# Kernel tuning notes

Measured on AMD Instinct MI355X. Metric: run time of the kernel, lower is better.

The kernel has to match this reference:

```python
import jax, jax.numpy as jnp
import numpy as np

HIDDEN = 1024
NUM_HEADS = 8
HEAD_DIM = HIDDEN // NUM_HEADS
ROPE_BASE = 10000.0
RMS_EPS = 1e-6


def _rotate_half(x):
    # interleaved rotate: (x0,x1,x2,x3,...) -> (-x1,x0,-x3,x2,...)
    x1 = x[..., ::2]
    x2 = x[..., 1::2]
    return jnp.stack([-x2, x1], axis=-1).reshape(x.shape)


def _rope_cos_sin(seq_len, rotary_dim, dtype):
    inv_freq = 1.0 / (ROPE_BASE ** (jnp.arange(0, rotary_dim, 2, dtype=jnp.float32) / rotary_dim))
    pos = jnp.arange(seq_len, dtype=jnp.float32)
    freqs = pos[:, None] * inv_freq[None, :]            # [S, rd/2]
    cos = jnp.repeat(jnp.cos(freqs), 2, axis=-1)        # [S, rd]
    sin = jnp.repeat(jnp.sin(freqs), 2, axis=-1)
    return cos.astype(dtype)[None, None], sin.astype(dtype)[None, None]


def setup_inputs() -> dict:
    key = jax.random.key(0)
    k = jax.random.split(key, 8)
    B, S, H = 2, 2048, HIDDEN
    hidden_states = jax.random.normal(k[0], (B, S, H), dtype=jnp.float32)
    attention_mask = jax.random.randint(k[1], (B, S, S), 0, 2) > 0
    rel_ts_bias = jax.random.normal(k[2], (B, S, S), dtype=jnp.float32)
    s1 = 1.0 / np.sqrt(H)
    W_qkvu = jax.random.normal(k[3], (H, H * 6), dtype=jnp.float32) * s1
    W_out = jax.random.normal(k[4], (H * 3, H), dtype=jnp.float32) * (1.0 / np.sqrt(H * 3))
    b_out = jnp.zeros((H,), dtype=jnp.float32)
    rms_weight = jnp.ones((H,), dtype=jnp.float32)
    return {"hidden_states": hidden_states, "attention_mask": attention_mask,
            "rel_ts_bias": rel_ts_bias, "W_qkvu": W_qkvu, "W_out": W_out,
            "b_out": b_out, "rms_weight": rms_weight}


def reference(hidden_states, attention_mask, rel_ts_bias, W_qkvu, W_out, b_out, rms_weight):
    B, S, H = hidden_states.shape
    nh, hd = NUM_HEADS, HEAD_DIM
    fused = jax.nn.silu(hidden_states @ W_qkvu)          # [B,S,6H]
    gated = fused[..., :3 * H]                            # [B,S,3H]
    v = fused[..., 3 * H:4 * H].reshape(B, S, nh, hd).transpose(0, 2, 1, 3)
    q = fused[..., 4 * H:5 * H].reshape(B, S, nh, hd).transpose(0, 2, 1, 3)
    kk = fused[..., 5 * H:].reshape(B, S, nh, hd).transpose(0, 2, 1, 3)

    cos, sin = _rope_cos_sin(S, hd, hidden_states.dtype)  # rotary_dim == head_dim
    q_rope = q * cos + _rotate_half(q) * sin
    k_rope = kk * cos + _rotate_half(kk) * sin

    inv_s = 1.0 / max(S, 1)
    qk = jax.nn.relu(jnp.einsum('bhnd,bhmd->bhnm', q, kk)) * inv_s
    qk_rope = jax.nn.relu(jnp.einsum('bhnd,bhmd->bhnm', q_rope, k_rope)) * inv_s

    mask = attention_mask[:, None]                        # [B,1,S,S]
    qk = jnp.where(mask, qk, 0.0)
    qk_rope = jnp.where(mask, qk_rope, 0.0)
    ts_bias = jnp.where(attention_mask, rel_ts_bias, 0.0)

    ts_out = jnp.einsum('bnm,bhmd->bnhd', ts_bias, v)
    rope_out = jnp.einsum('bhnm,bhmd->bnhd', qk_rope, v)
    plain_out = jnp.einsum('bhnm,bhmd->bnhd', qk, v)

    combined = jnp.concatenate([rope_out, ts_out, plain_out], axis=-1).reshape(B, S, 3 * H)
    out = (combined * gated) @ W_out + b_out
    y = out + hidden_states
    rms = jax.lax.rsqrt(jnp.mean(y * y, axis=-1, keepdims=True) + RMS_EPS)
    return y * rms * rms_weight
```

## Files before the change

### kernel.cpp

```cpp
#include <hip/hip_runtime.h>
#include <math.h>

static constexpr int Bz = 2;
static constexpr int Sq = 2048;
static constexpr int Hh = 1024;
static constexpr int NH = 8;
static constexpr int HD = 128;
static constexpr int H3 = 3072;
static constexpr int H6 = 6144;

typedef unsigned short ushort_t;
typedef float f32x4v __attribute__((ext_vector_type(4)));
typedef float f32x16v __attribute__((ext_vector_type(16)));
typedef short s16x8 __attribute__((ext_vector_type(8)));

static constexpr size_t FUSED_OFF = 0;
static constexpr size_t A2_OFF    = 12582912;
static constexpr size_t HB_OFF    = 18874368;
static constexpr size_t MTB_OFF   = 18874368;
static constexpr size_t WQT_OFF   = 20971520;
static constexpr size_t WOT_OFF   = 24117248;
static constexpr size_t QR_OFF    = 25690112;
static constexpr size_t KR_OFF    = 27787264;
static constexpr size_t VT_OFF    = 29884416;
static constexpr size_t TAB_OFF   = 31981568;
static constexpr size_t FLAG_OFF  = 32243712;
static constexpr size_t TSB_OFF   = 32243716;

__device__ __forceinline__ float silu_(float x) { return x / (1.0f + expf(-x)); }
__device__ __forceinline__ ushort_t f2bf(float x) {
  unsigned int u = __float_as_uint(x);
  u += 0x7fffu + ((u >> 16) & 1u);
  return (ushort_t)(u >> 16);
}
__device__ __forceinline__ float bf2f(ushort_t u) {
  return __uint_as_float(((unsigned int)u) << 16);
}
__device__ __forceinline__ void g2l16(const ushort_t* g, ushort_t* l) {
  __builtin_amdgcn_global_load_lds(
      (const __attribute__((address_space(1))) unsigned int*)g,
      (__attribute__((address_space(3))) unsigned int*)l, 16, 0, 0);
}

__global__ __launch_bounds__(256) void hstu_mask_detect(const unsigned int* __restrict__ m,
                                                        int* __restrict__ flag) {
  __shared__ int s_any;
  if (threadIdx.x == 0) s_any = 0;
  __syncthreads();
  int any = 0;
  for (int i = threadIdx.x; i < 65536; i += 256)
    if (m[i] > 1u) any = 1;
  if (any) s_any = 1;
  __syncthreads();
  if (threadIdx.x == 0) *flag = s_any;
}

__global__ __launch_bounds__(256) void hstu_tab(float* __restrict__ tab) {
  int t = blockIdx.x * 256 + threadIdx.x;
  int i = t & 63;
  int s = t >> 6;
  float inv = powf(10000.0f, -(float)i / 64.0f);
  float sn, cs;
  sincosf((float)s * inv, &sn, &cs);
  tab[2 * t + 0] = cs;
  tab[2 * t + 1] = sn;
}

__global__ __launch_bounds__(256) void hstu_msk(const int* __restrict__ mask32,
                                                const unsigned char* __restrict__ mask8,
                                                const int* __restrict__ mflag,
                                                const float* __restrict__ bias,
                                                ushort_t* __restrict__ tsb,
                                                unsigned char* __restrict__ mtb8) {
  const size_t base = ((size_t)blockIdx.x * 256 + threadIdx.x) * 8;
  const int m_u8 = *mflag;
  int mk[8];
  if (m_u8) {
    uchar4 a = *(const uchar4*)&mask8[base];
    uchar4 b = *(const uchar4*)&mask8[base + 4];
    mk[0] = a.x; mk[1] = a.y; mk[2] = a.z; mk[3] = a.w;
    mk[4] = b.x; mk[5] = b.y; mk[6] = b.z; mk[7] = b.w;
  } else {
    int4 a = *(const int4*)&mask32[base];
    int4 b = *(const int4*)&mask32[base + 4];
    mk[0] = a.x; mk[1] = a.y; mk[2] = a.z; mk[3] = a.w;
    mk[4] = b.x; mk[5] = b.y; mk[6] = b.z; mk[7] = b.w;
  }
  float4 b0 = *(const float4*)&bias[base];
  float4 b1 = *(const float4*)&bias[base + 4];
  float bb[8] = {b0.x, b0.y, b0.z, b0.w, b1.x, b1.y, b1.z, b1.w};
  ushort_t ts[8];
  unsigned char mo[8];
#pragma unroll
  for (int i = 0; i < 8; ++i) {
    ts[i] = f2bf(mk[i] ? bb[i] : 0.0f);
    mo[i] = mk[i] ? 1u : 0u;
  }
  *(s16x8*)&tsb[base] = *(s16x8*)ts;
  *(uint2*)&mtb8[base] = *(uint2*)mo;
}

__global__ __launch_bounds__(256) void hstu_cvt(const float* __restrict__ in,
                                                ushort_t* __restrict__ out, int n4) {
  int i = blockIdx.x * 256 + threadIdx.x;
  if (i >= n4) return;
  float4 v = *(const float4*)&in[(size_t)i * 4];
  ushort4 o;
  o.x = f2bf(v.x); o.y = f2bf(v.y); o.z = f2bf(v.z); o.w = f2bf(v.w);
  *(ushort4*)&out[(size_t)i * 4] = o;
}

__global__ __launch_bounds__(256) void hstu_cvt_t(const float* __restrict__ in,
                                                  ushort_t* __restrict__ out, int K, int N) {
  __shared__ float t[32][33];
  const int n0 = blockIdx.x * 32, k0 = blockIdx.y * 32;
  const int c = threadIdx.x & 31, rr = threadIdx.x >> 5;
#pragma unroll
  for (int p = 0; p < 4; ++p)
    t[rr + p * 8][c] = in[(size_t)(k0 + rr + p * 8) * N + n0 + c];
  __syncthreads();
#pragma unroll
  for (int p = 0; p < 4; ++p)
    out[(size_t)(n0 + rr + p * 8) * K + k0 + c] = f2bf(t[c][rr + p * 8]);
}

__global__ __launch_bounds__(256) void hstu_rope(const ushort_t* __restrict__ fused,
                                                 const float2* __restrict__ tab,
                                                 ushort_t* __restrict__ qr,
                                                 ushort_t* __restrict__ kr) {
  const int idx = blockIdx.x * 256 + threadIdx.x;
  const int row = idx >> 7;
  const int cg = (idx & 127) * 8;
  const int s = row & (Sq - 1);
  const float2* trow = &tab[(size_t)s * 64 + ((cg & 127) >> 1)];
  float2 t[4];
#pragma unroll
  for (int p = 0; p < 4; ++p) t[p] = trow[p];

  s16x8 q8 = *(const s16x8*)&fused[(size_t)row * H6 + 4 * Hh + cg];
  s16x8 k8 = *(const s16x8*)&fused[(size_t)row * H6 + 5 * Hh + cg];
  ushort_t qo[8], ko[8];
#pragma unroll
  for (int p = 0; p < 4; ++p) {
    float qx = bf2f((ushort_t)q8[2 * p]), qy = bf2f((ushort_t)q8[2 * p + 1]);
    float kx = bf2f((ushort_t)k8[2 * p]), ky = bf2f((ushort_t)k8[2 * p + 1]);
    qo[2 * p] = f2bf(qx * t[p].x - qy * t[p].y);
    qo[2 * p + 1] = f2bf(qy * t[p].x + qx * t[p].y);
    ko[2 * p] = f2bf(kx * t[p].x - ky * t[p].y);
    ko[2 * p + 1] = f2bf(ky * t[p].x + kx * t[p].y);
  }
  *(s16x8*)&qr[(size_t)row * Hh + cg] = *(s16x8*)qo;
  *(s16x8*)&kr[(size_t)row * Hh + cg] = *(s16x8*)ko;
}

__global__ __launch_bounds__(256) void hstu_vt(const ushort_t* __restrict__ fused,
                                               ushort_t* __restrict__ vt) {
  __shared__ ushort_t t[32][36];
  const int m0 = blockIdx.x * 32, d0 = blockIdx.y * 32, bh = blockIdx.z;
  const int b = bh >> 3, h = bh & 7;
  const int r = threadIdx.x >> 3, cg = (threadIdx.x & 7) * 4;
  *(ushort4*)&t[r][cg] =
      *(const ushort4*)&fused[(size_t)(b * Sq + m0 + r) * H6 + 3 * Hh + h * HD + d0 + cg];
  __syncthreads();
  ushort4 o;
  o.x = t[cg + 0][r]; o.y = t[cg + 1][r]; o.z = t[cg + 2][r]; o.w = t[cg + 3][r];
  *(ushort4*)&vt[(size_t)(bh * HD + d0 + r) * Sq + m0 + cg] = o;
}

__global__ __launch_bounds__(256) void hstu_gemm_silu(const ushort_t* __restrict__ A,
                                                      const ushort_t* __restrict__ Bt,
                                                      ushort_t* __restrict__ C) {
  constexpr int K = 1024, N = H6;
  __shared__ ushort_t As[128 * 64];
  __shared__ ushort_t Bs[128 * 64];
  const int tid = threadIdx.x, lane = tid & 63, wid = tid >> 6;
  const int lo4 = lane & 15, hi2 = lane >> 4;
  const int wr = wid >> 1, wc = wid & 1;
  const int row0 = blockIdx.y * 128, col0 = blockIdx.x * 128;
  const int srow = lane >> 3, scol = (lane & 7) * 8;
  f32x4v acc[4][4];
#pragma unroll
  for (int i = 0; i < 4; ++i)
#pragma unroll
    for (int j = 0; j < 4; ++j) acc[i][j] = {0.f, 0.f, 0.f, 0.f};

  for (int k0 = 0; k0 < K; k0 += 64) {
    __syncthreads();
#pragma unroll
    for (int i = 0; i < 4; ++i) {
      const int rb = wid * 32 + i * 8;
      g2l16(&A[(size_t)(row0 + rb + srow) * K + k0 + scol], &As[rb * 64]);
      g2l16(&Bt[(size_t)(col0 + rb + srow) * K + k0 + scol], &Bs[rb * 64]);
    }
    __syncthreads();
#pragma unroll
    for (int kc = 0; kc < 2; ++kc) {
      s16x8 af[4], bfr[4];
#pragma unroll
      for (int mi = 0; mi < 4; ++mi)
        af[mi] = *(const s16x8*)&As[(wr * 64 + mi * 16 + lo4) * 64 + kc * 32 + hi2 * 8];
#pragma unroll
      for (int nj = 0; nj < 4; ++nj)
        bfr[nj] = *(const s16x8*)&Bs[(wc * 64 + nj * 16 + lo4) * 64 + kc * 32 + hi2 * 8];
#pragma unroll
      for (int mi = 0; mi < 4; ++mi)
#pragma unroll
        for (int nj = 0; nj < 4; ++nj)
          acc[mi][nj] = __builtin_amdgcn_mfma_f32_16x16x32_bf16(af[mi], bfr[nj], acc[mi][nj], 0, 0, 0);
    }
  }
#pragma unroll
  for (int mi = 0; mi < 4; ++mi)
#pragma unroll
    for (int nj = 0; nj < 4; ++nj)
#pragma unroll
      for (int r = 0; r < 4; ++r) {
        const int row = row0 + wr * 64 + mi * 16 + hi2 * 4 + r;
        const int col = col0 + wc * 64 + nj * 16 + lo4;
        C[(size_t)row * N + col] = f2bf(silu_(acc[mi][nj][r]));
      }
}

__global__ __launch_bounds__(256) void hstu_gemm_out(const ushort_t* __restrict__ A,
                                                     const ushort_t* __restrict__ Bt,
                                                     const float* __restrict__ bout,
                                                     const float* __restrict__ hidden,
                                                     float* __restrict__ C) {
  constexpr int K = H3, N = Hh;
  __shared__ ushort_t As[128 * 64];
  __shared__ ushort_t Bs[64 * 64];
  const int tid = threadIdx.x, lane = tid & 63, wid = tid >> 6;
  const int lo4 = lane & 15, hi2 = lane >> 4;
  const int wr = wid >> 1, wc = wid & 1;
  const int row0 = blockIdx.y * 128, col0 = blockIdx.x * 64;
  const int srow = lane >> 3, scol = (lane & 7) * 8;
  f32x4v acc[4][2];
#pragma unroll
  for (int i = 0; i < 4; ++i)
#pragma unroll
    for (int j = 0; j < 2; ++j) acc[i][j] = {0.f, 0.f, 0.f, 0.f};

  for (int k0 = 0; k0 < K; k0 += 64) {
    __syncthreads();
#pragma unroll
    for (int i = 0; i < 4; ++i) {
      const int rb = wid * 32 + i * 8;
      g2l16(&A[(size_t)(row0 + rb + srow) * K + k0 + scol], &As[rb * 64]);
    }
#pragma unroll
    for (int i = 0; i < 2; ++i) {
      const int rb = wid * 16 + i * 8;
      g2l16(&Bt[(size_t)(col0 + rb + srow) * K + k0 + scol], &Bs[rb * 64]);
    }
    __syncthreads();
#pragma unroll
    for (int kc = 0; kc < 2; ++kc) {
      s16x8 af[4], bfr[2];
#pragma unroll
      for (int mi = 0; mi < 4; ++mi)
        af[mi] = *(const s16x8*)&As[(wr * 64 + mi * 16 + lo4) * 64 + kc * 32 + hi2 * 8];
#pragma unroll
      for (int nj = 0; nj < 2; ++nj)
        bfr[nj] = *(const s16x8*)&Bs[(wc * 32 + nj * 16 + lo4) * 64 + kc * 32 + hi2 * 8];
#pragma unroll
      for (int mi = 0; mi < 4; ++mi)
#pragma unroll
        for (int nj = 0; nj < 2; ++nj)
          acc[mi][nj] = __builtin_amdgcn_mfma_f32_16x16x32_bf16(af[mi], bfr[nj], acc[mi][nj], 0, 0, 0);
    }
  }
#pragma unroll
  for (int mi = 0; mi < 4; ++mi)
#pragma unroll
    for (int nj = 0; nj < 2; ++nj)
#pragma unroll
      for (int r = 0; r < 4; ++r) {
        const int row = row0 + wr * 64 + mi * 16 + hi2 * 4 + r;
        const int col = col0 + wc * 32 + nj * 16 + lo4;
        C[(size_t)row * N + col] = acc[mi][nj][r] + bout[col] + hidden[(size_t)row * N + col];
      }
}

__global__ __launch_bounds__(512, 4) void hstu_attn(const ushort_t* __restrict__ fused,
                                                    const ushort_t* __restrict__ qr,
                                                    const ushort_t* __restrict__ kr,
                                                    const ushort_t* __restrict__ vt,
                                                    const ushort_t* __restrict__ tsb,
                                                    const unsigned char* __restrict__ mtb8,
                                                    ushort_t* __restrict__ a2) {
  __shared__ __align__(16) ushort_t Ks[64][136];
  __shared__ __align__(16) ushort_t KRs[64][136];
  __shared__ __align__(16) ushort_t Vt[128][72];
  __shared__ __align__(16) ushort_t Pl[2][64][72];
  __shared__ __align__(16) unsigned char Mt[64][72];

  const int tid = threadIdx.x;
  const int lane = tid & 63;
  const int wid = tid >> 6;
  const int l31 = lane & 31;
  const int khalf = lane >> 5;
  const int h = blockIdx.x;
  const int n0 = blockIdx.y * 64;
  const int b = blockIdx.z;
  const float ivs = 1.0f / 2048.0f;
  constexpr int NT = Sq / 64;

  const int t_w = wid >> 2;
  const int nq = (wid >> 1) & 1;
  const int mq = wid & 1;
  const int nh = wid & 1;
  const int dq = wid >> 1;

#define STAGE_QQR()                                                              \
  {                                                                              \
    _Pragma("unroll") for (int p = 0; p < 2; ++p) {                              \
      const int row = (tid >> 4) + p * 32;                                       \
      const int col = (tid & 15) * 8;                                            \
      const size_t gr = (size_t)(b * Sq + n0 + row);                             \
      *(s16x8*)&Ks[row][col] = *(const s16x8*)&fused[gr * H6 + 4 * Hh + h * HD + col]; \
      *(s16x8*)&KRs[row][col] = *(const s16x8*)&qr[gr * Hh + h * HD + col];      \
    }                                                                            \
  }
#define STAGE_KKR(T)                                                             \
  {                                                                              \
    _Pragma("unroll") for (int p = 0; p < 2; ++p) {                              \
      const int row = (tid >> 4) + p * 32;                                       \
      const int col = (tid & 15) * 8;                                            \
      const size_t gr = (size_t)(b * Sq + (T) * 64 + row);                       \
      *(s16x8*)&Ks[row][col] = *(const s16x8*)&fused[gr * H6 + 5 * Hh + h * HD + col]; \
      *(s16x8*)&KRs[row][col] = *(const s16x8*)&kr[gr * Hh + h * HD + col];      \
    }                                                                            \
  }
#define STAGE_MT(T)                                                              \
  {                                                                              \
    const int row = tid >> 3;                                                    \
    const int c8 = (tid & 7) * 8;                                                \
    *(uint2*)&Mt[row][c8] =                                                      \
        *(const uint2*)&mtb8[(size_t)(b * Sq + n0 + row) * Sq + (T) * 64 + c8];  \
  }
#define STAGE_VT(T)                                                              \
  {                                                                              \
    _Pragma("unroll") for (int p = 0; p < 2; ++p) {                              \
      const int dd = (tid >> 3) + p * 64;                                        \
      const int mcol = (tid & 7) * 8;                                            \
      *(s16x8*)&Vt[dd][mcol] =                                                   \
          *(const s16x8*)&vt[(size_t)((b * NH + h) * HD + dd) * Sq + (T) * 64 + mcol]; \
    }                                                                            \
  }

  STAGE_QQR();
  __syncthreads();
  s16x8 qf[8];
  {
    const ushort_t(*Qsrc)[136] = t_w ? KRs : Ks;
#pragma unroll
    for (int ks = 0; ks < 8; ++ks)
      qf[ks] = *(const s16x8*)&Qsrc[nq * 32 + l31][ks * 16 + khalf * 8];
  }
  __syncthreads();
  STAGE_KKR(0);
  STAGE_MT(0);
  __syncthreads();

  f32x16v acc0 = {0.f, 0.f, 0.f, 0.f, 0.f, 0.f, 0.f, 0.f,
                  0.f, 0.f, 0.f, 0.f, 0.f, 0.f, 0.f, 0.f};
  f32x16v acc1 = acc0;
  f32x16v acc2 = acc0;

  const size_t tsrow = (size_t)(b * Sq + n0 + nh * 32 + l31) * Sq;

  for (int t = 0; t < NT; ++t) {
    const int m0 = t * 64;
    STAGE_VT(t);
    s16x8 tsf[4];
#pragma unroll
    for (int ks = 0; ks < 4; ++ks)
      tsf[ks] = *(const s16x8*)&tsb[tsrow + m0 + ks * 16 + khalf * 8];
    {
      const ushort_t(*Kmat)[136] = t_w ? KRs : Ks;
      f32x16v sacc = {0.f, 0.f, 0.f, 0.f, 0.f, 0.f, 0.f, 0.f,
                      0.f, 0.f, 0.f, 0.f, 0.f, 0.f, 0.f, 0.f};
#pragma unroll
      for (int ks = 0; ks < 8; ++ks) {
        s16x8 bfr = *(const s16x8*)&Kmat[mq * 32 + l31][ks * 16 + khalf * 8];
        sacc = __builtin_amdgcn_mfma_f32_32x32x16_bf16(qf[ks], bfr, sacc, 0, 0, 0);
      }
      const int m = mq * 32 + l31;
#pragma unroll
      for (int r = 0; r < 16; ++r) {
        const int n = nq * 32 + (r & 3) + 8 * (r >> 2) + 4 * khalf;
        const float val = Mt[n][m] ? fmaxf(sacc[r], 0.f) * ivs : 0.f;
        Pl[t_w][n][m] = f2bf(val);
      }
    }
    __syncthreads();
    if (t + 1 < NT) {
      STAGE_KKR(t + 1);
      STAGE_MT(t + 1);
    }
#pragma unroll
    for (int ks = 0; ks < 4; ++ks) {
      s16x8 bV = *(const s16x8*)&Vt[dq * 32 + l31][ks * 16 + khalf * 8];
      s16x8 aP0 = *(const s16x8*)&Pl[0][nh * 32 + l31][ks * 16 + khalf * 8];
      s16x8 aP1 = *(const s16x8*)&Pl[1][nh * 32 + l31][ks * 16 + khalf * 8];
      acc0 = __builtin_amdgcn_mfma_f32_32x32x16_bf16(aP0, bV, acc0, 0, 0, 0);
      acc1 = __builtin_amdgcn_mfma_f32_32x32x16_bf16(aP1, bV, acc1, 0, 0, 0);
      acc2 = __builtin_amdgcn_mfma_f32_32x32x16_bf16(tsf[ks], bV, acc2, 0, 0, 0);
    }
    __syncthreads();
  }
#undef STAGE_QQR
#undef STAGE_KKR
#undef STAGE_MT
#undef STAGE_VT

  const int dd = dq * 32 + l31;
#pragma unroll
  for (int r = 0; r < 16; ++r) {
    const int n = n0 + nh * 32 + (r & 3) + 8 * (r >> 2) + 4 * khalf;
    const size_t rowb = (size_t)(b * Sq + n);
    const int c_pl = h * 384 + 256 + dd;
    const int c_ro = h * 384 + 0 + dd;
    const int c_ts = h * 384 + 128 + dd;
    a2[rowb * H3 + c_pl] = f2bf(acc0[r] * bf2f(fused[rowb * H6 + c_pl]));
    a2[rowb * H3 + c_ro] = f2bf(acc1[r] * bf2f(fused[rowb * H6 + c_ro]));
    a2[rowb * H3 + c_ts] = f2bf(acc2[r] * bf2f(fused[rowb * H6 + c_ts]));
  }
}

__global__ __launch_bounds__(256) void hstu_rms(float* __restrict__ y,
                                                const float* __restrict__ w) {
  __shared__ float red[4];
  const int row = blockIdx.x;
  const int tid = threadIdx.x;
  float4 v = *(float4*)&y[(size_t)row * Hh + tid * 4];
  float ss = v.x * v.x + v.y * v.y + v.z * v.z + v.w * v.w;
#pragma unroll
  for (int o = 32; o > 0; o >>= 1) ss += __shfl_down(ss, o);
  if ((tid & 63) == 0) red[tid >> 6] = ss;
  __syncthreads();
  const float tot = red[0] + red[1] + red[2] + red[3];
  const float r = 1.0f / sqrtf(tot / (float)Hh + 1e-6f);
  float4 wv = *(const float4*)&w[tid * 4];
  v.x *= r * wv.x;
  v.y *= r * wv.y;
  v.z *= r * wv.z;
  v.w *= r * wv.w;
  *(float4*)&y[(size_t)row * Hh + tid * 4] = v;
}

extern "C" void kernel_launch(void* const* d_in, const int* in_sizes, int n_in,
                              void* d_out, int out_size, void* d_ws, size_t ws_size,
                              hipStream_t stream) {
  const float* hidden = (const float*)d_in[0];
  const void* mask = d_in[1];
  const float* bias = (const float*)d_in[2];
  const float* Wqkvu = (const float*)d_in[3];
  const float* Wout = (const float*)d_in[4];
  const float* bout = (const float*)d_in[5];
  const float* rmsw = (const float*)d_in[6];
  float* out = (float*)d_out;
  float* ws = (float*)d_ws;

  ushort_t* fused = (ushort_t*)(ws + FUSED_OFF);
  ushort_t* a2 = (ushort_t*)(ws + A2_OFF);
  ushort_t* hb = (ushort_t*)(ws + HB_OFF);
  unsigned char* mtb8 = (unsigned char*)(ws + MTB_OFF);
  ushort_t* wqt = (ushort_t*)(ws + WQT_OFF);
  ushort_t* wot = (ushort_t*)(ws + WOT_OFF);
  ushort_t* qrb = (ushort_t*)(ws + QR_OFF);
  ushort_t* krb = (ushort_t*)(ws + KR_OFF);
  ushort_t* vtb = (ushort_t*)(ws + VT_OFF);
  float* tab = ws + TAB_OFF;
  int* mflag = (int*)(ws + FLAG_OFF);
  ushort_t* tsbp = (ushort_t*)(ws + TSB_OFF);

  hstu_mask_detect<<<1, 256, 0, stream>>>((const unsigned int*)mask, mflag);
  hstu_tab<<<512, 256, 0, stream>>>(tab);
  hstu_cvt<<<4096, 256, 0, stream>>>(hidden, hb, (Bz * Sq * Hh) / 4);
  hstu_cvt_t<<<dim3(H6 / 32, Hh / 32), 256, 0, stream>>>(Wqkvu, wqt, Hh, H6);
  hstu_cvt_t<<<dim3(Hh / 32, H3 / 32), 256, 0, stream>>>(Wout, wot, H3, Hh);
  hstu_gemm_silu<<<dim3(H6 / 128, (Bz * Sq) / 128), 256, 0, stream>>>(hb, wqt, fused);
  hstu_msk<<<(Bz * Sq * Sq / 8) / 256, 256, 0, stream>>>(
      (const int*)mask, (const unsigned char*)mask, mflag, bias, tsbp, mtb8);
  hstu_rope<<<(Bz * Sq * Hh / 8) / 256, 256, 0, stream>>>(fused, (const float2*)tab, qrb, krb);
  hstu_vt<<<dim3(Sq / 32, HD / 32, Bz * NH), 256, 0, stream>>>(fused, vtb);
  hstu_attn<<<dim3(NH, Sq / 64, Bz), 512, 0, stream>>>(fused, qrb, krb, vtb, tsbp, mtb8, a2);
  hstu_gemm_out<<<dim3(Hh / 64, (Bz * Sq) / 128), 256, 0, stream>>>(a2, wot, bout, hidden, out);
  hstu_rms<<<Bz * Sq, 256, 0, stream>>>(out, rmsw);
}
```

Before: 371.3 us.

## Bit-pack attention mask and transpose score MFMA for packed bf16 P stores

The mask is now packed into one bit per element instead of one byte, and the attention kernel reads a 32-bit word per lane straight from global memory rather than staging a byte tile in LDS. The score MFMA swaps its operands so each lane holds consecutive key columns for one query row. That lets P be written with packed bf16 conversions as 8-byte stores instead of scalar 2-byte scattered stores. This is meant to cut mask bandwidth and LDS traffic, at the cost of a dependent global load of the mask bits each iteration.

```diff
diff --git a/kernel.cpp b/kernel.cpp
--- a/kernel.cpp
+++ b/kernel.cpp
@@ -17,7 +17,7 @@
 static constexpr size_t FUSED_OFF = 0;
 static constexpr size_t A2_OFF    = 12582912;
 static constexpr size_t HB_OFF    = 18874368;
-static constexpr size_t MTB_OFF   = 18874368;
+static constexpr size_t MBITS_OFF = 18874368;
 static constexpr size_t WQT_OFF   = 20971520;
 static constexpr size_t WOT_OFF   = 24117248;
 static constexpr size_t QR_OFF    = 25690112;
@@ -35,6 +35,11 @@
 }
 __device__ __forceinline__ float bf2f(ushort_t u) {
   return __uint_as_float(((unsigned int)u) << 16);
+}
+__device__ __forceinline__ unsigned int cvt_pk_bf16(float lo, float hi) {
+  unsigned int r;
+  asm("v_cvt_pk_bf16_f32 %0, %1, %2" : "=v"(r) : "v"(lo), "v"(hi));
+  return r;
 }
 __device__ __forceinline__ void g2l16(const ushort_t* g, ushort_t* l) {
   __builtin_amdgcn_global_load_lds(
@@ -71,8 +76,9 @@
                                                 const int* __restrict__ mflag,
                                                 const float* __restrict__ bias,
                                                 ushort_t* __restrict__ tsb,
-                                                unsigned char* __restrict__ mtb8) {
-  const size_t base = ((size_t)blockIdx.x * 256 + threadIdx.x) * 8;
+                                                unsigned char* __restrict__ mbits) {
+  const size_t idx = (size_t)blockIdx.x * 256 + threadIdx.x;
+  const size_t base = idx * 8;
   const int m_u8 = *mflag;
   int mk[8];
   if (m_u8) {
@@ -90,14 +96,14 @@
   float4 b1 = *(const float4*)&bias[base + 4];
   float bb[8] = {b0.x, b0.y, b0.z, b0.w, b1.x, b1.y, b1.z, b1.w};
   ushort_t ts[8];
-  unsigned char mo[8];
+  unsigned int byte = 0;
 #pragma unroll
   for (int i = 0; i < 8; ++i) {
     ts[i] = f2bf(mk[i] ? bb[i] : 0.0f);
-    mo[i] = mk[i] ? 1u : 0u;
+    byte |= (mk[i] ? 1u : 0u) << i;
   }
   *(s16x8*)&tsb[base] = *(s16x8*)ts;
-  *(uint2*)&mtb8[base] = *(uint2*)mo;
+  mbits[idx] = (unsigned char)byte;
 }
 
 __global__ __launch_bounds__(256) void hstu_cvt(const float* __restrict__ in,
@@ -286,13 +292,12 @@
                                                     const ushort_t* __restrict__ kr,
                                                     const ushort_t* __restrict__ vt,
                                                     const ushort_t* __restrict__ tsb,
-                                                    const unsigned char* __restrict__ mtb8,
+                                                    const unsigned int* __restrict__ mbits32,
                                                     ushort_t* __restrict__ a2) {
   __shared__ __align__(16) ushort_t Ks[64][136];
   __shared__ __align__(16) ushort_t KRs[64][136];
   __shared__ __align__(16) ushort_t Vt[128][72];
   __shared__ __align__(16) ushort_t Pl[2][64][72];
-  __shared__ __align__(16) unsigned char Mt[64][72];
 
   const int tid = threadIdx.x;
   const int lane = tid & 63;
@@ -331,13 +336,6 @@
       *(s16x8*)&KRs[row][col] = *(const s16x8*)&kr[gr * Hh + h * HD + col];      \
     }                                                                            \
   }
-#define STAGE_MT(T)                                                              \
-  {                                                                              \
-    const int row = tid >> 3;                                                    \
-    const int c8 = (tid & 7) * 8;                                                \
-    *(uint2*)&Mt[row][c8] =                                                      \
-        *(const uint2*)&mtb8[(size_t)(b * Sq + n0 + row) * Sq + (T) * 64 + c8];  \
-  }
 #define STAGE_VT(T)                                                              \
   {                                                                              \
     _Pragma("unroll") for (int p = 0; p < 2; ++p) {                              \
@@ -359,7 +357,6 @@
   }
   __syncthreads();
   STAGE_KKR(0);
-  STAGE_MT(0);
   __syncthreads();
 
   f32x16v acc0 = {0.f, 0.f, 0.f, 0.f, 0.f, 0.f, 0.f, 0.f,
@@ -368,6 +365,7 @@
   f32x16v acc2 = acc0;
 
   const size_t tsrow = (size_t)(b * Sq + n0 + nh * 32 + l31) * Sq;
+  const size_t mrow = (size_t)(b * Sq + n0 + nq * 32 + l31) * 64;
 
   for (int t = 0; t < NT; ++t) {
     const int m0 = t * 64;
@@ -376,28 +374,34 @@
 #pragma unroll
     for (int ks = 0; ks < 4; ++ks)
       tsf[ks] = *(const s16x8*)&tsb[tsrow + m0 + ks * 16 + khalf * 8];
+    const unsigned int bits = mbits32[mrow + t * 2 + mq];
     {
       const ushort_t(*Kmat)[136] = t_w ? KRs : Ks;
       f32x16v sacc = {0.f, 0.f, 0.f, 0.f, 0.f, 0.f, 0.f, 0.f,
                       0.f, 0.f, 0.f, 0.f, 0.f, 0.f, 0.f, 0.f};
 #pragma unroll
       for (int ks = 0; ks < 8; ++ks) {
-        s16x8 bfr = *(const s16x8*)&Kmat[mq * 32 + l31][ks * 16 + khalf * 8];
-        sacc = __builtin_amdgcn_mfma_f32_32x32x16_bf16(qf[ks], bfr, sacc, 0, 0, 0);
+        s16x8 kf = *(const s16x8*)&Kmat[mq * 32 + l31][ks * 16 + khalf * 8];
+        sacc = __builtin_amdgcn_mfma_f32_32x32x16_bf16(kf, qf[ks], sacc, 0, 0, 0);
       }
-      const int m = mq * 32 + l31;
-#pragma unroll
-      for (int r = 0; r < 16; ++r) {
-        const int n = nq * 32 + (r & 3) + 8 * (r >> 2) + 4 * khalf;
-        const float val = Mt[n][m] ? fmaxf(sacc[r], 0.f) * ivs : 0.f;
-        Pl[t_w][n][m] = f2bf(val);
+      const int n_loc = nq * 32 + l31;
+#pragma unroll
+      for (int i = 0; i < 4; ++i) {
+        float v[4];
+#pragma unroll
+        for (int j = 0; j < 4; ++j) {
+          const int mu = 8 * i + 4 * khalf + j;
+          const float x = fmaxf(sacc[4 * i + j], 0.f) * ivs;
+          v[j] = ((bits >> mu) & 1u) ? x : 0.f;
+        }
+        uint2 pk;
+        pk.x = cvt_pk_bf16(v[0], v[1]);
+        pk.y = cvt_pk_bf16(v[2], v[3]);
+        *(uint2*)&Pl[t_w][n_loc][mq * 32 + 8 * i + 4 * khalf] = pk;
       }
     }
     __syncthreads();
-    if (t + 1 < NT) {
-      STAGE_KKR(t + 1);
-      STAGE_MT(t + 1);
-    }
+    if (t + 1 < NT) STAGE_KKR(t + 1);
 #pragma unroll
     for (int ks = 0; ks < 4; ++ks) {
       s16x8 bV = *(const s16x8*)&Vt[dq * 32 + l31][ks * 16 + khalf * 8];
@@ -411,7 +415,6 @@
   }
 #undef STAGE_QQR
 #undef STAGE_KKR
-#undef STAGE_MT
 #undef STAGE_VT
 
   const int dd = dq * 32 + l31;
@@ -465,7 +468,7 @@
   ushort_t* fused = (ushort_t*)(ws + FUSED_OFF);
   ushort_t* a2 = (ushort_t*)(ws + A2_OFF);
   ushort_t* hb = (ushort_t*)(ws + HB_OFF);
-  unsigned char* mtb8 = (unsigned char*)(ws + MTB_OFF);
+  unsigned char* mbits = (unsigned char*)(ws + MBITS_OFF);
   ushort_t* wqt = (ushort_t*)(ws + WQT_OFF);
   ushort_t* wot = (ushort_t*)(ws + WOT_OFF);
   ushort_t* qrb = (ushort_t*)(ws + QR_OFF);
@@ -482,10 +485,11 @@
   hstu_cvt_t<<<dim3(Hh / 32, H3 / 32), 256, 0, stream>>>(Wout, wot, H3, Hh);
   hstu_gemm_silu<<<dim3(H6 / 128, (Bz * Sq) / 128), 256, 0, stream>>>(hb, wqt, fused);
   hstu_msk<<<(Bz * Sq * Sq / 8) / 256, 256, 0, stream>>>(
-      (const int*)mask, (const unsigned char*)mask, mflag, bias, tsbp, mtb8);
+      (const int*)mask, (const unsigned char*)mask, mflag, bias, tsbp, mbits);
   hstu_rope<<<(Bz * Sq * Hh / 8) / 256, 256, 0, stream>>>(fused, (const float2*)tab, qrb, krb);
   hstu_vt<<<dim3(Sq / 32, HD / 32, Bz * NH), 256, 0, stream>>>(fused, vtb);
-  hstu_attn<<<dim3(NH, Sq / 64, Bz), 512, 0, stream>>>(fused, qrb, krb, vtb, tsbp, mtb8, a2);
+  hstu_attn<<<dim3(NH, Sq / 64, Bz), 512, 0, stream>>>(
+      fused, qrb, krb, vtb, tsbp, (const unsigned int*)mbits, a2);
   hstu_gemm_out<<<dim3(Hh / 64, (Bz * Sq) / 128), 256, 0, stream>>>(a2, wot, bout, hidden, out);
   hstu_rms<<<Bz * Sq, 256, 0, stream>>>(out, rmsw);
 }
```

Result: slower. 508.2 us (+36.9%).
